# Kernel optimization log

Measured on AMD Instinct MI355X. Metric: run time of the kernel, lower is better.

Reference implementation:

```python
import jax, jax.numpy as jnp
import numpy as np

FEAT_STRIDE = 16
PRE_NMS_TOP_N = 4000   # cfg[cfg_key].RPN_PRE_NMS_TOP_N
POST_NMS_TOP_N = 300   # cfg[cfg_key].RPN_POST_NMS_TOP_N
NMS_THRESH = 0.7       # cfg[cfg_key].RPN_NMS_THRESH


def _generate_anchors(base_size=16, ratios=(0.5, 1.0, 2.0), scales=(8, 16, 32)):
    ratios = np.array(ratios, dtype=np.float64)
    scales = np.array(scales, dtype=np.float64)
    base = np.array([1, 1, base_size, base_size], dtype=np.float64) - 1

    def whctrs(a):
        w = a[2] - a[0] + 1
        h = a[3] - a[1] + 1
        return w, h, a[0] + 0.5 * (w - 1), a[1] + 0.5 * (h - 1)

    def mk(ws, hs, xc, yc):
        ws = np.atleast_1d(ws)[:, None]
        hs = np.atleast_1d(hs)[:, None]
        return np.hstack((xc - 0.5 * (ws - 1), yc - 0.5 * (hs - 1),
                          xc + 0.5 * (ws - 1), yc + 0.5 * (hs - 1)))

    w, h, xc, yc = whctrs(base)
    size = w * h
    ws = np.round(np.sqrt(size / ratios))
    hs = np.round(ws * ratios)
    ratio_anchors = mk(ws, hs, xc, yc)
    out = []
    for i in range(ratio_anchors.shape[0]):
        w, h, xc, yc = whctrs(ratio_anchors[i])
        out.append(mk(w * scales, h * scales, xc, yc))
    return np.vstack(out).astype(np.float32)  # [9,4]


def _nms_keep(boxes, thresh):
    # boxes sorted by score desc, [N,4]; torchvision-style IoU (no +1).
    x1, y1, x2, y2 = boxes[:, 0], boxes[:, 1], boxes[:, 2], boxes[:, 3]
    areas = (x2 - x1) * (y2 - y1)
    lt = jnp.maximum(boxes[:, None, :2], boxes[None, :, :2])
    rb = jnp.minimum(boxes[:, None, 2:], boxes[None, :, 2:])
    wh = jnp.clip(rb - lt, 0.0)
    inter = wh[..., 0] * wh[..., 1]
    iou = inter / (areas[:, None] + areas[None, :] - inter + 1e-9)  # [N,N]
    N = boxes.shape[0]
    idx = jnp.arange(N)
    def body(i, keep):
        sup = (iou[i] > thresh) & (idx > i) & keep[i]
        return keep & ~sup
    return jax.lax.fori_loop(0, N, body, jnp.ones((N,), jnp.bool_))


def _per_image(boxes, scores):
    # pre-NMS top-k by score (matches sort-desc + slice)
    _, order = jax.lax.top_k(scores, PRE_NMS_TOP_N)
    b = boxes[order]
    keep = _nms_keep(jax.lax.stop_gradient(b), NMS_THRESH)
    rank = jnp.cumsum(keep) - 1                       # position among kept
    tgt = jnp.where(keep, rank, POST_NMS_TOP_N)       # OOB indices are dropped
    return jnp.zeros((POST_NMS_TOP_N, 4), boxes.dtype).at[tgt].set(b, mode='drop')


def reference(scores, bbox_deltas, im_info, anchors):
    B, A, H, W = scores.shape
    # anchor shifts over the feature grid
    sx = jnp.arange(W, dtype=scores.dtype) * FEAT_STRIDE
    sy = jnp.arange(H, dtype=scores.dtype) * FEAT_STRIDE
    yy, xx = jnp.meshgrid(sy, sx, indexing='ij')
    shifts = jnp.stack([xx.ravel(), yy.ravel(), xx.ravel(), yy.ravel()], axis=1)  # [K,4]
    all_anchors = (anchors[None, :, :] + shifts[:, None, :]).reshape(-1, 4)       # [K*A,4]

    deltas = bbox_deltas.transpose(0, 2, 3, 1).reshape(B, -1, 4)  # [B,K*A,4]
    sc = scores.transpose(0, 2, 3, 1).reshape(B, -1)              # [B,K*A]

    # bbox_transform_inv
    w = all_anchors[:, 2] - all_anchors[:, 0] + 1.0
    h = all_anchors[:, 3] - all_anchors[:, 1] + 1.0
    cx = all_anchors[:, 0] + 0.5 * w
    cy = all_anchors[:, 1] + 0.5 * h
    pcx = deltas[..., 0] * w + cx
    pcy = deltas[..., 1] * h + cy
    pw = jnp.exp(deltas[..., 2]) * w
    ph = jnp.exp(deltas[..., 3]) * h
    props = jnp.stack([pcx - 0.5 * pw, pcy - 0.5 * ph,
                       pcx + 0.5 * pw, pcy + 0.5 * ph], axis=-1)  # [B,K*A,4]

    # clip_boxes: x in [0, im_w-1], y in [0, im_h-1]
    hi = jnp.stack([im_info[:, 1] - 1, im_info[:, 0] - 1,
                    im_info[:, 1] - 1, im_info[:, 0] - 1], axis=1)  # [B,4]
    props = jnp.clip(props, 0.0, hi[:, None, :])

    boxes_out = jax.vmap(_per_image)(props, sc)  # [B,POST,4]
    batch_col = jnp.broadcast_to(
        jnp.arange(B, dtype=scores.dtype)[:, None, None], (B, POST_NMS_TOP_N, 1))
    return jnp.concatenate([batch_col, boxes_out], axis=-1)  # [B,POST,5]


def setup_inputs():
    key = jax.random.key(0)
    k1, k2 = jax.random.split(key)
    B, A, H, W = 4, 9, 50, 76
    scores = jax.random.normal(k1, (B, A, H, W), jnp.float32)
    bbox_deltas = jax.random.normal(k2, (B, 4 * A, H, W), jnp.float32) * 0.2
    im_info = jnp.tile(jnp.array([[800.0, 1216.0, 1.0]], jnp.float32), (B, 1))
    anchors = jnp.asarray(_generate_anchors())
    return {"scores": scores, "bbox_deltas": bbox_deltas,
            "im_info": im_info, "anchors": anchors}
```

## Files before the change

### kernel.cpp

```cpp
#include <hip/hip_runtime.h>
#include <stdint.h>

#define A_N 9
#define H_N 50
#define W_N 76
#define HW_N (H_N * W_N)
#define N_PROP (A_N * HW_N)
#define B_N 4
#define PRE_NMS 4000
#define POST_NMS 300
#define NMS_TH 0.7f
#define SORT_N 4096
#define MASK_WORDS 64
#define CAND_MAX 5120
#define NBINS 4096
#define NPAIR 32
#define NLW 5
#define DEC_BLKS ((N_PROP + 255) / 256)

__global__ __launch_bounds__(256) void decode_kernel(
    const float* __restrict__ scores,
    const float* __restrict__ deltas,
    const float* __restrict__ im_info,
    const float* __restrict__ anchors,
    float4* __restrict__ boxes,
    unsigned long long* __restrict__ keys,
    unsigned* __restrict__ ghist) {
#pragma clang fp contract(off)
    __shared__ unsigned hist[NBINS];
    int tid = threadIdx.x;
    int b = blockIdx.y;
    int r = blockIdx.x * 256 + tid;
#pragma unroll
    for (int i = 0; i < NBINS / 256; ++i) hist[tid + i * 256] = 0u;
    __syncthreads();

    if (r < N_PROP) {
        int a = r / HW_N;
        int hw = r - a * HW_N;
        int hy = hw / W_N;
        int wx = hw - hy * W_N;

        float sx = (float)wx * 16.0f;
        float sy = (float)hy * 16.0f;
        float ax1 = anchors[a * 4 + 0] + sx;
        float ay1 = anchors[a * 4 + 1] + sy;
        float ax2 = anchors[a * 4 + 2] + sx;
        float ay2 = anchors[a * 4 + 3] + sy;
        float aw = ax2 - ax1 + 1.0f;
        float ah = ay2 - ay1 + 1.0f;
        float cx = ax1 + 0.5f * aw;
        float cy = ay1 + 0.5f * ah;

        const float* db = deltas + ((size_t)b * 36 + (size_t)a * 4) * HW_N + hw;
        float d0 = db[0];
        float d1 = db[HW_N];
        float d2 = db[2 * HW_N];
        float d3 = db[3 * HW_N];

        float pcx = d0 * aw + cx;
        float pcy = d1 * ah + cy;
        float pw  = expf(d2) * aw;
        float ph  = expf(d3) * ah;

        float x1 = pcx - 0.5f * pw;
        float y1 = pcy - 0.5f * ph;
        float x2 = pcx + 0.5f * pw;
        float y2 = pcy + 0.5f * ph;

        float xhi = im_info[b * 3 + 1] - 1.0f;
        float yhi = im_info[b * 3 + 0] - 1.0f;
        x1 = fminf(fmaxf(x1, 0.0f), xhi);
        y1 = fminf(fmaxf(y1, 0.0f), yhi);
        x2 = fminf(fmaxf(x2, 0.0f), xhi);
        y2 = fminf(fmaxf(y2, 0.0f), yhi);

        boxes[(size_t)b * N_PROP + r] = make_float4(x1, y1, x2, y2);

        float s = scores[((size_t)b * A_N + a) * HW_N + hw];
        unsigned f = __float_as_uint(s);
        unsigned sk = f ^ ((f & 0x80000000u) ? 0xFFFFFFFFu : 0x80000000u);
        unsigned n_ref = (unsigned)(hw * A_N + a);
        unsigned long long key = ((unsigned long long)sk << 32) | (unsigned)(~n_ref);
        keys[(size_t)b * N_PROP + r] = key;
        atomicAdd(&hist[(unsigned)(key >> 52)], 1u);
    }
    __syncthreads();
#pragma unroll
    for (int i = 0; i < NBINS / 256; ++i) {
        unsigned v = hist[tid + i * 256];
        if (v) atomicAdd(&ghist[b * NBINS + tid + i * 256], v);
    }
}

__global__ __launch_bounds__(64) void findT_kernel(const unsigned* __restrict__ ghist,
                                                   int* __restrict__ Tout) {
    __shared__ unsigned h[NBINS];
    int b = blockIdx.x;
    int lane = threadIdx.x;
    for (int i = lane; i < NBINS; i += 64) h[i] = ghist[b * NBINS + i];
    __syncthreads();
    unsigned gsum = 0;
    for (int j = 0; j < 64; ++j) gsum += h[lane * 64 + j];
    unsigned s = gsum;
    for (int d = 1; d < 64; d <<= 1) {
        unsigned t = (unsigned)__shfl_down((int)s, d);
        if (lane + d < 64) s += t;
    }
    unsigned long long bal = __ballot(s >= PRE_NMS);
    int gstar = 63 - __builtin_clzll(bal);
    unsigned after = (gstar < 63) ? (unsigned)__builtin_amdgcn_readlane((int)s, gstar + 1) : 0u;
    unsigned R = PRE_NMS - after;
    unsigned s2 = h[gstar * 64 + lane];
    for (int d = 1; d < 64; d <<= 1) {
        unsigned t = (unsigned)__shfl_down((int)s2, d);
        if (lane + d < 64) s2 += t;
    }
    unsigned long long bal2 = __ballot(s2 >= R);
    int j = 63 - __builtin_clzll(bal2);
    if (lane == 0) Tout[b] = gstar * 64 + j;
}

__global__ void compact_kernel(const unsigned long long* __restrict__ keys,
                               const int* __restrict__ T,
                               unsigned* __restrict__ cnt,
                               unsigned long long* __restrict__ cand) {
    int b = blockIdx.y;
    int n = blockIdx.x * 256 + threadIdx.x;
    bool pred = false;
    unsigned long long k = 0ull;
    if (n < N_PROP) {
        k = keys[(size_t)b * N_PROP + n];
        pred = ((int)(unsigned)(k >> 52) >= T[b]);
    }
    unsigned long long m = __ballot(pred);
    if (m) {
        int lane = threadIdx.x & 63;
        int lead = __ffsll((unsigned long long)m) - 1;
        unsigned base = 0;
        if (lane == lead) base = atomicAdd(&cnt[b], (unsigned)__popcll(m));
        base = __shfl((int)base, lead);
        if (pred) {
            unsigned pos = base + (unsigned)__popcll(m & ((1ull << lane) - 1ull));
            if (pos < CAND_MAX) cand[(size_t)b * CAND_MAX + pos] = k;
        }
    }
}

__global__ __launch_bounds__(256) void rank_scatter_kernel(
    const unsigned long long* __restrict__ cand,
    const unsigned* __restrict__ cnt,
    const float4* __restrict__ boxes,
    float4* __restrict__ sortedBoxes) {
    __shared__ unsigned long long sk[256];
    int b = blockIdx.y;
    int tid = threadIdx.x;
    int ci = blockIdx.x * 64 + (tid >> 2);
    int q = tid & 3;
    int mc = (int)min(cnt[b], (unsigned)CAND_MAX);
    unsigned long long my = (ci < mc) ? cand[(size_t)b * CAND_MAX + ci] : 0ull;
    int rank = 0;
    int nt = (mc + 255) >> 8;
    for (int t = 0; t < nt; ++t) {
        int j = t * 256 + tid;
        sk[tid] = (j < mc) ? cand[(size_t)b * CAND_MAX + j] : 0ull;
        __syncthreads();
#pragma unroll 16
        for (int c = 0; c < 64; ++c) {
            int cc = q * 64 + ((c + q * 17) & 63);
            rank += (sk[cc] > my) ? 1 : 0;
        }
        __syncthreads();
    }
    rank += __shfl_xor(rank, 1);
    rank += __shfl_xor(rank, 2);
    if (q == 0 && ci < mc && rank < PRE_NMS) {
        unsigned n_ref = ~(unsigned)(my & 0xFFFFFFFFull);
        unsigned a = n_ref % A_N;
        unsigned hw = n_ref / A_N;
        sortedBoxes[(size_t)b * SORT_N + rank] =
            boxes[(size_t)b * N_PROP + a * HW_N + hw];
    }
    if (q == 1) {
        int pi = blockIdx.x * 64 + (tid >> 2);
        if (pi >= PRE_NMS && pi < SORT_N)
            sortedBoxes[(size_t)b * SORT_N + pi] = make_float4(0.f, 0.f, 0.f, 0.f);
    }
}

__global__ __launch_bounds__(256) void iou_mask_kernel(
    const float4* __restrict__ sortedBoxes,
    unsigned long long* __restrict__ colmaj,
    unsigned long long* __restrict__ rowmaj) {
#pragma clang fp contract(off)
    int b = blockIdx.y;
    int wv = threadIdx.x >> 6;
    int t = threadIdx.x & 63;
    int k = blockIdx.x * 4 + wv;
    int rc = 0;
    while (k >= 64 - rc) { k -= 64 - rc; ++rc; }
    int cc = rc + k;

    __shared__ float4 colb[4][64];
    colb[wv][t] = sortedBoxes[(size_t)b * SORT_N + cc * 64 + t];
    __syncthreads();

    int r = rc * 64 + t;
    float4 rb = sortedBoxes[(size_t)b * SORT_N + r];
    float rarea = (rb.z - rb.x) * (rb.w - rb.y);
    unsigned long long word = 0ull;
    for (int c = 0; c < 64; ++c) {
        int j = cc * 64 + c;
        float4 cb = colb[wv][c];
        float carea = (cb.z - cb.x) * (cb.w - cb.y);
        float ltx = fmaxf(rb.x, cb.x);
        float lty = fmaxf(rb.y, cb.y);
        float rbx = fminf(rb.z, cb.z);
        float rby = fminf(rb.w, cb.w);
        float iw = fmaxf(rbx - ltx, 0.0f);
        float ih = fmaxf(rby - lty, 0.0f);
        float inter = iw * ih;
        float iou = inter / (rarea + carea - inter + 1e-9f);
        if (iou > NMS_TH && j > r) word |= (1ull << c);
    }
    colmaj[((size_t)b * MASK_WORDS + cc) * SORT_N + r] = word;
    rowmaj[((size_t)b * SORT_N + r) * MASK_WORDS + cc] = word;
}

__device__ __forceinline__ unsigned long long rl64(unsigned long long v, int src) {
    unsigned lo = (unsigned)__builtin_amdgcn_readlane((int)(unsigned)(v & 0xFFFFFFFFull), src);
    unsigned hi = (unsigned)__builtin_amdgcn_readlane((int)(unsigned)(v >> 32), src);
    return ((unsigned long long)hi << 32) | lo;
}

__device__ __forceinline__ unsigned long long redor64(unsigned long long alive,
                                                      unsigned long long v, int lane) {
    unsigned long long x = ((alive >> lane) & 1ull) ? v : 0ull;
    x |= __shfl_xor(x, 1);
    x |= __shfl_xor(x, 2);
    x |= __shfl_xor(x, 4);
    x |= __shfl_xor(x, 8);
    x |= __shfl_xor(x, 16);
    x |= __shfl_xor(x, 32);
    return x;
}

__device__ __forceinline__ void block_sync() {
    asm volatile("s_waitcnt lgkmcnt(0)" ::: "memory");
    __builtin_amdgcn_s_barrier();
    asm volatile("" ::: "memory");
}

#define GLOAD(dst, addr) \
    asm volatile("global_load_dwordx2 %0, %1, off" : "=v"(dst) : "v"(addr))
#define WAITV0 asm volatile("s_waitcnt vmcnt(0)" ::: "memory")
#define SCHED0 __builtin_amdgcn_sched_barrier(0)

#define TILE_COL(P, t) ((t) < 6 ? 2 * (P) + (t) : 2 * (P) + 1 + ((t) - 6))
#define TILE_RB(P, t)  ((size_t)((t) < 6 ? 2 * (P) : 2 * (P) + 1) << 6)
#define TILE_ADDR(P, t) \
    (C + (size_t)(TILE_COL(P, t) < 64 ? TILE_COL(P, t) : 63) * SORT_N + TILE_RB(P, t) + lane)

#define ISSUE_PAIR(P)                                                          \
    do {                                                                       \
        pf_vmask = 0u;                                                         \
        GLOAD(pf0,  TILE_ADDR(P, 0));  if (TILE_COL(P, 0)  < 64) pf_vmask |= 1u << 0;  \
        GLOAD(pf1,  TILE_ADDR(P, 1));  if (TILE_COL(P, 1)  < 64) pf_vmask |= 1u << 1;  \
        GLOAD(pf2,  TILE_ADDR(P, 2));  if (TILE_COL(P, 2)  < 64) pf_vmask |= 1u << 2;  \
        GLOAD(pf3,  TILE_ADDR(P, 3));  if (TILE_COL(P, 3)  < 64) pf_vmask |= 1u << 3;  \
        GLOAD(pf4,  TILE_ADDR(P, 4));  if (TILE_COL(P, 4)  < 64) pf_vmask |= 1u << 4;  \
        GLOAD(pf5,  TILE_ADDR(P, 5));  if (TILE_COL(P, 5)  < 64) pf_vmask |= 1u << 5;  \
        GLOAD(pf6,  TILE_ADDR(P, 6));  if (TILE_COL(P, 6)  < 64) pf_vmask |= 1u << 6;  \
        GLOAD(pf7,  TILE_ADDR(P, 7));  if (TILE_COL(P, 7)  < 64) pf_vmask |= 1u << 7;  \
        GLOAD(pf8,  TILE_ADDR(P, 8));  if (TILE_COL(P, 8)  < 64) pf_vmask |= 1u << 8;  \
        GLOAD(pf9,  TILE_ADDR(P, 9));  if (TILE_COL(P, 9)  < 64) pf_vmask |= 1u << 9;  \
        GLOAD(pf10, TILE_ADDR(P, 10)); if (TILE_COL(P, 10) < 64) pf_vmask |= 1u << 10; \
    } while (0)

#define NEXTROW2(rk)                                                           \
    int rk;                                                                    \
    {                                                                          \
        if (xA) { int bb_ = __builtin_ctzll(xA); xA &= xA - 1; rk = baseA + bb_; } \
        else if (xB) { int bb_ = __builtin_ctzll(xB); xB &= xB - 1; rk = baseB + bb_; } \
        else rk = rpad;                                                        \
    }

__global__ __launch_bounds__(512, 1) void nms_scan_kernel(
    const unsigned long long* __restrict__ colmaj,
    const unsigned long long* __restrict__ rowmaj,
    const float4* __restrict__ sortedBoxes,
    float* __restrict__ out) {
    int b = blockIdx.x;
    int tid = threadIdx.x;
    int lane = tid & 63;
    int wv = tid >> 6;
    const unsigned long long* C = colmaj + (size_t)b * MASK_WORDS * SORT_N;
    const unsigned long long* R = rowmaj + (size_t)b * SORT_N * MASK_WORDS;

    __shared__ int kept[POST_NMS];
    __shared__ unsigned remW[MASK_WORDS][2];
    __shared__ unsigned long long aliveLds[MASK_WORDS];
    __shared__ unsigned long long ring[4][11][64];
    __shared__ unsigned long long car2[2][2];
    __shared__ int doneLds;
    __shared__ int kcntLds;

    if (tid < MASK_WORDS) { remW[tid][0] = 0u; remW[tid][1] = 0u; aliveLds[tid] = 0ull; }
    if (tid < 4) car2[tid >> 1][tid & 1] = 0ull;
    if (tid == 0) { doneLds = 0; kcntLds = 0; }

    unsigned long long pf0=0,pf1=0,pf2=0,pf3=0,pf4=0,pf5=0,pf6=0,pf7=0,pf8=0,pf9=0,pf10=0;
    unsigned pf_vmask = 0u;
    bool pf_have = false;
    unsigned long long gp0=0,gp1=0,gp2=0,gp3=0,gp4=0,gp5=0,gp6=0,gp7=0;
    bool ld_valid = false;

    if (wv == 1) {
        for (int t = 0; t < 11; ++t) {
            int col = TILE_COL(0, t);
            unsigned long long v =
                (col < 64) ? C[(size_t)col * SORT_N + TILE_RB(0, t) + lane] : 0ull;
            ring[0][t][lane] = v;
        }
        ISSUE_PAIR(1);
        pf_have = true;
    }
    block_sync();

    unsigned long long carA = 0ull, carB = 0ull;
    int kcnt = 0;

    for (int q = 0; q < NPAIR; ++q) {
        if (wv == 0) {
            int A = 2 * q, Bg = A + 1, slot = q & 3;
            unsigned long long dA  = ring[slot][0][lane];
            unsigned long long tA1 = ring[slot][1][lane];
            unsigned long long tA2 = ring[slot][2][lane];
            unsigned long long tA3 = ring[slot][3][lane];
            unsigned long long dB  = ring[slot][6][lane];
            unsigned long long tB1 = ring[slot][7][lane];
            unsigned long long tB2 = ring[slot][8][lane];
            unsigned long long remA =
                ((unsigned long long)remW[A][1] << 32) | (unsigned long long)remW[A][0];
            unsigned long long remB =
                ((unsigned long long)remW[Bg][1] << 32) | (unsigned long long)remW[Bg][0];
            unsigned long long h2A = car2[q & 1][0];
            unsigned long long h2B = car2[q & 1][1];
            bool hit = false;
            unsigned long long aliveA = 0ull, aliveB = 0ull;
            unsigned long long pend = ~(remA | carA | h2A);
            while (pend) {
                int bit = __builtin_ctzll(pend);
                if (lane == 0) kept[kcnt] = (A << 6) + bit;
                ++kcnt;
                aliveA |= 1ull << bit;
                if (kcnt == POST_NMS) { hit = true; break; }
                pend &= ~(rl64(dA, bit) | (1ull << bit));
            }
            if (!hit) {
                unsigned long long nA1 = redor64(aliveA, tA1, lane);
                pend = ~(remB | carB | h2B | nA1);
                while (pend) {
                    int bit = __builtin_ctzll(pend);
                    if (lane == 0) kept[kcnt] = (Bg << 6) + bit;
                    ++kcnt;
                    aliveB |= 1ull << bit;
                    if (kcnt == POST_NMS) { hit = true; break; }
                    pend &= ~(rl64(dB, bit) | (1ull << bit));
                }
            }
            carA = redor64(aliveA, tA2, lane) | redor64(aliveB, tB1, lane);
            carB = redor64(aliveA, tA3, lane) | redor64(aliveB, tB2, lane);
            if (lane == 0) {
                aliveLds[A]  = aliveA;
                aliveLds[Bg] = aliveB;
                kcntLds = kcnt;
                if (hit) doneLds = 1;
            }
        } else if (wv == 1) {
            if (pf_have) {
                WAITV0;
                SCHED0;
                int wp = q + 1;
                if (wp < NPAIR) {
                    int ws = wp & 3;
                    ring[ws][0][lane]  = (pf_vmask & (1u << 0))  ? pf0  : 0ull;
                    ring[ws][1][lane]  = (pf_vmask & (1u << 1))  ? pf1  : 0ull;
                    ring[ws][2][lane]  = (pf_vmask & (1u << 2))  ? pf2  : 0ull;
                    ring[ws][3][lane]  = (pf_vmask & (1u << 3))  ? pf3  : 0ull;
                    ring[ws][4][lane]  = (pf_vmask & (1u << 4))  ? pf4  : 0ull;
                    ring[ws][5][lane]  = (pf_vmask & (1u << 5))  ? pf5  : 0ull;
                    ring[ws][6][lane]  = (pf_vmask & (1u << 6))  ? pf6  : 0ull;
                    ring[ws][7][lane]  = (pf_vmask & (1u << 7))  ? pf7  : 0ull;
                    ring[ws][8][lane]  = (pf_vmask & (1u << 8))  ? pf8  : 0ull;
                    ring[ws][9][lane]  = (pf_vmask & (1u << 9))  ? pf9  : 0ull;
                    ring[ws][10][lane] = (pf_vmask & (1u << 10)) ? pf10 : 0ull;
                }
                pf_have = false;
            }
            int ip = q + 2;
            if (ip < NPAIR) {
                ISSUE_PAIR(ip);
                pf_have = true;
            }
        } else if (wv == 2) {
            if (q >= 1) {
                int p = q - 1, sp = p & 3;
                unsigned long long aA = aliveLds[2 * p];
                unsigned long long aB = aliveLds[2 * p + 1];
                unsigned long long tA4 = ring[sp][4][lane];
                unsigned long long tA5 = ring[sp][5][lane];
                unsigned long long tB3 = ring[sp][9][lane];
                unsigned long long tB4 = ring[sp][10][lane];
                unsigned long long c0 = redor64(aA, tA4, lane) | redor64(aB, tB3, lane);
                unsigned long long c1 = redor64(aA, tA5, lane) | redor64(aB, tB4, lane);
                if (lane == 0) {
                    car2[(q + 1) & 1][0] = c0;
                    car2[(q + 1) & 1][1] = c1;
                }
            }
        } else {
            if (ld_valid) {
                WAITV0;
                SCHED0;
                unsigned long long acc =
                    ((gp0 | gp1) | (gp2 | gp3)) | ((gp4 | gp5) | (gp6 | gp7));
                unsigned lo = (unsigned)acc, hi = (unsigned)(acc >> 32);
                if (lo) atomicOr(&remW[lane][0], lo);
                if (hi) atomicOr(&remW[lane][1], hi);
                ld_valid = false;
            }
            if (q >= 1) {
                int p = q - 1, gA = 2 * p, gB = 2 * p + 1;
                unsigned long long aA = aliveLds[gA];
                unsigned long long aB = aliveLds[gB];
                int k = wv - 3;
                unsigned long long below = (1ull << lane) - 1ull;
                bool inA = (aA >> lane) & 1ull;
                bool inB = (aB >> lane) & 1ull;
                int posA = (int)__popcll(aA & below);
                int posB = (int)__popcll(aA) + (int)__popcll(aB & below);
                unsigned long long mA = __ballot(inA && (posA % NLW) == k);
                unsigned long long mB = __ballot(inB && (posB % NLW) == k);
                if (mA | mB) {
                    int baseA = gA << 6, baseB = gB << 6;
                    unsigned long long xA = mA, xB = mB;
                    int rpad = mA ? (baseA + __builtin_ctzll(mA))
                                  : (baseB + __builtin_ctzll(mB));
                    NEXTROW2(r0) NEXTROW2(r1) NEXTROW2(r2) NEXTROW2(r3)
                    NEXTROW2(r4) NEXTROW2(r5) NEXTROW2(r6) NEXTROW2(r7)
                    const unsigned long long* Rb = R + lane;
                    GLOAD(gp0, Rb + (size_t)r0 * MASK_WORDS);
                    GLOAD(gp1, Rb + (size_t)r1 * MASK_WORDS);
                    GLOAD(gp2, Rb + (size_t)r2 * MASK_WORDS);
                    GLOAD(gp3, Rb + (size_t)r3 * MASK_WORDS);
                    GLOAD(gp4, Rb + (size_t)r4 * MASK_WORDS);
                    GLOAD(gp5, Rb + (size_t)r5 * MASK_WORDS);
                    GLOAD(gp6, Rb + (size_t)r6 * MASK_WORDS);
                    GLOAD(gp7, Rb + (size_t)r7 * MASK_WORDS);
                    ld_valid = true;
                    unsigned long long ovf = 0ull;
                    while (xA) {
                        int bb = __builtin_ctzll(xA); xA &= xA - 1;
                        ovf |= Rb[(size_t)(baseA + bb) * MASK_WORDS];
                    }
                    while (xB) {
                        int bb = __builtin_ctzll(xB); xB &= xB - 1;
                        ovf |= Rb[(size_t)(baseB + bb) * MASK_WORDS];
                    }
                    if (ovf) {
                        unsigned lo = (unsigned)ovf, hi = (unsigned)(ovf >> 32);
                        if (lo) atomicOr(&remW[lane][0], lo);
                        if (hi) atomicOr(&remW[lane][1], hi);
                    }
                }
            }
        }
        block_sync();
        if (doneLds) break;
    }

    WAITV0;
    __syncthreads();

    int kc = kcntLds;
    for (int r = tid; r < POST_NMS; r += 512) {
        float* o = out + ((size_t)b * POST_NMS + r) * 5;
        float4 bx = make_float4(0.f, 0.f, 0.f, 0.f);
        if (r < kc) bx = sortedBoxes[(size_t)b * SORT_N + kept[r]];
        o[0] = (float)b;
        o[1] = bx.x;
        o[2] = bx.y;
        o[3] = bx.z;
        o[4] = bx.w;
    }
}

extern "C" void kernel_launch(void* const* d_in, const int* in_sizes, int n_in,
                              void* d_out, int out_size, void* d_ws, size_t ws_size,
                              hipStream_t stream) {
    const float* scores  = (const float*)d_in[0];
    const float* deltas  = (const float*)d_in[1];
    const float* im_info = (const float*)d_in[2];
    const float* anchors = (const float*)d_in[3];
    float* out = (float*)d_out;

    char* ws = (char*)d_ws;
    size_t off = 0;
    float4* boxes = (float4*)(ws + off);
    off += (size_t)B_N * N_PROP * sizeof(float4);
    off = (off + 255) & ~(size_t)255;
    unsigned long long* keys = (unsigned long long*)(ws + off);
    off += (size_t)B_N * N_PROP * sizeof(unsigned long long);
    off = (off + 255) & ~(size_t)255;
    float4* sortedBoxes = (float4*)(ws + off);
    off += (size_t)B_N * SORT_N * sizeof(float4);
    off = (off + 255) & ~(size_t)255;
    unsigned long long* colmaj = (unsigned long long*)(ws + off);
    off += (size_t)B_N * MASK_WORDS * SORT_N * sizeof(unsigned long long);
    off = (off + 255) & ~(size_t)255;
    unsigned long long* rowmaj = (unsigned long long*)(ws + off);
    off += (size_t)B_N * SORT_N * MASK_WORDS * sizeof(unsigned long long);
    off = (off + 255) & ~(size_t)255;
    unsigned long long* cand = (unsigned long long*)(ws + off);
    off += (size_t)B_N * CAND_MAX * sizeof(unsigned long long);
    off = (off + 255) & ~(size_t)255;
    unsigned* ghist = (unsigned*)(ws + off);
    size_t zero_off = off;
    off += (size_t)B_N * NBINS * sizeof(unsigned);
    unsigned* cnt = (unsigned*)(ws + off);
    off += (size_t)B_N * sizeof(unsigned);
    size_t zero_bytes = off - zero_off;
    off = (off + 255) & ~(size_t)255;
    int* Tbuf = (int*)(ws + off);
    off += (size_t)B_N * sizeof(int);

    hipMemsetAsync((void*)ghist, 0, zero_bytes, stream);

    decode_kernel<<<dim3(DEC_BLKS, B_N), 256, 0, stream>>>(
        scores, deltas, im_info, anchors, boxes, keys, ghist);
    findT_kernel<<<B_N, 64, 0, stream>>>(ghist, Tbuf);
    compact_kernel<<<dim3((N_PROP + 255) / 256, B_N), 256, 0, stream>>>(
        keys, Tbuf, cnt, cand);
    rank_scatter_kernel<<<dim3(CAND_MAX / 64, B_N), 256, 0, stream>>>(
        cand, cnt, boxes, sortedBoxes);
    iou_mask_kernel<<<dim3(520, B_N), 256, 0, stream>>>(sortedBoxes, colmaj, rowmaj);
    nms_scan_kernel<<<B_N, 512, 0, stream>>>(colmaj, rowmaj, sortedBoxes, out);
}
```

Before: 214.5 us.

## Fuse all pipeline stages into one cooperative persistent kernel with grid syncs

```diff
diff --git a/kernel.cpp b/kernel.cpp
--- a/kernel.cpp
+++ b/kernel.cpp
@@ -1,5 +1,8 @@
 #include <hip/hip_runtime.h>
+#include <hip/hip_cooperative_groups.h>
 #include <stdint.h>
+
+namespace cg = cooperative_groups;
 
 #define A_N 9
 #define H_N 50
@@ -15,217 +18,9 @@
 #define CAND_MAX 5120
 #define NBINS 4096
 #define NPAIR 32
-#define NLW 5
 #define DEC_BLKS ((N_PROP + 255) / 256)
-
-__global__ __launch_bounds__(256) void decode_kernel(
-    const float* __restrict__ scores,
-    const float* __restrict__ deltas,
-    const float* __restrict__ im_info,
-    const float* __restrict__ anchors,
-    float4* __restrict__ boxes,
-    unsigned long long* __restrict__ keys,
-    unsigned* __restrict__ ghist) {
-#pragma clang fp contract(off)
-    __shared__ unsigned hist[NBINS];
-    int tid = threadIdx.x;
-    int b = blockIdx.y;
-    int r = blockIdx.x * 256 + tid;
-#pragma unroll
-    for (int i = 0; i < NBINS / 256; ++i) hist[tid + i * 256] = 0u;
-    __syncthreads();
-
-    if (r < N_PROP) {
-        int a = r / HW_N;
-        int hw = r - a * HW_N;
-        int hy = hw / W_N;
-        int wx = hw - hy * W_N;
-
-        float sx = (float)wx * 16.0f;
-        float sy = (float)hy * 16.0f;
-        float ax1 = anchors[a * 4 + 0] + sx;
-        float ay1 = anchors[a * 4 + 1] + sy;
-        float ax2 = anchors[a * 4 + 2] + sx;
-        float ay2 = anchors[a * 4 + 3] + sy;
-        float aw = ax2 - ax1 + 1.0f;
-        float ah = ay2 - ay1 + 1.0f;
-        float cx = ax1 + 0.5f * aw;
-        float cy = ay1 + 0.5f * ah;
-
-        const float* db = deltas + ((size_t)b * 36 + (size_t)a * 4) * HW_N + hw;
-        float d0 = db[0];
-        float d1 = db[HW_N];
-        float d2 = db[2 * HW_N];
-        float d3 = db[3 * HW_N];
-
-        float pcx = d0 * aw + cx;
-        float pcy = d1 * ah + cy;
-        float pw  = expf(d2) * aw;
-        float ph  = expf(d3) * ah;
-
-        float x1 = pcx - 0.5f * pw;
-        float y1 = pcy - 0.5f * ph;
-        float x2 = pcx + 0.5f * pw;
-        float y2 = pcy + 0.5f * ph;
-
-        float xhi = im_info[b * 3 + 1] - 1.0f;
-        float yhi = im_info[b * 3 + 0] - 1.0f;
-        x1 = fminf(fmaxf(x1, 0.0f), xhi);
-        y1 = fminf(fmaxf(y1, 0.0f), yhi);
-        x2 = fminf(fmaxf(x2, 0.0f), xhi);
-        y2 = fminf(fmaxf(y2, 0.0f), yhi);
-
-        boxes[(size_t)b * N_PROP + r] = make_float4(x1, y1, x2, y2);
-
-        float s = scores[((size_t)b * A_N + a) * HW_N + hw];
-        unsigned f = __float_as_uint(s);
-        unsigned sk = f ^ ((f & 0x80000000u) ? 0xFFFFFFFFu : 0x80000000u);
-        unsigned n_ref = (unsigned)(hw * A_N + a);
-        unsigned long long key = ((unsigned long long)sk << 32) | (unsigned)(~n_ref);
-        keys[(size_t)b * N_PROP + r] = key;
-        atomicAdd(&hist[(unsigned)(key >> 52)], 1u);
-    }
-    __syncthreads();
-#pragma unroll
-    for (int i = 0; i < NBINS / 256; ++i) {
-        unsigned v = hist[tid + i * 256];
-        if (v) atomicAdd(&ghist[b * NBINS + tid + i * 256], v);
-    }
-}
-
-__global__ __launch_bounds__(64) void findT_kernel(const unsigned* __restrict__ ghist,
-                                                   int* __restrict__ Tout) {
-    __shared__ unsigned h[NBINS];
-    int b = blockIdx.x;
-    int lane = threadIdx.x;
-    for (int i = lane; i < NBINS; i += 64) h[i] = ghist[b * NBINS + i];
-    __syncthreads();
-    unsigned gsum = 0;
-    for (int j = 0; j < 64; ++j) gsum += h[lane * 64 + j];
-    unsigned s = gsum;
-    for (int d = 1; d < 64; d <<= 1) {
-        unsigned t = (unsigned)__shfl_down((int)s, d);
-        if (lane + d < 64) s += t;
-    }
-    unsigned long long bal = __ballot(s >= PRE_NMS);
-    int gstar = 63 - __builtin_clzll(bal);
-    unsigned after = (gstar < 63) ? (unsigned)__builtin_amdgcn_readlane((int)s, gstar + 1) : 0u;
-    unsigned R = PRE_NMS - after;
-    unsigned s2 = h[gstar * 64 + lane];
-    for (int d = 1; d < 64; d <<= 1) {
-        unsigned t = (unsigned)__shfl_down((int)s2, d);
-        if (lane + d < 64) s2 += t;
-    }
-    unsigned long long bal2 = __ballot(s2 >= R);
-    int j = 63 - __builtin_clzll(bal2);
-    if (lane == 0) Tout[b] = gstar * 64 + j;
-}
-
-__global__ void compact_kernel(const unsigned long long* __restrict__ keys,
-                               const int* __restrict__ T,
-                               unsigned* __restrict__ cnt,
-                               unsigned long long* __restrict__ cand) {
-    int b = blockIdx.y;
-    int n = blockIdx.x * 256 + threadIdx.x;
-    bool pred = false;
-    unsigned long long k = 0ull;
-    if (n < N_PROP) {
-        k = keys[(size_t)b * N_PROP + n];
-        pred = ((int)(unsigned)(k >> 52) >= T[b]);
-    }
-    unsigned long long m = __ballot(pred);
-    if (m) {
-        int lane = threadIdx.x & 63;
-        int lead = __ffsll((unsigned long long)m) - 1;
-        unsigned base = 0;
-        if (lane == lead) base = atomicAdd(&cnt[b], (unsigned)__popcll(m));
-        base = __shfl((int)base, lead);
-        if (pred) {
-            unsigned pos = base + (unsigned)__popcll(m & ((1ull << lane) - 1ull));
-            if (pos < CAND_MAX) cand[(size_t)b * CAND_MAX + pos] = k;
-        }
-    }
-}
-
-__global__ __launch_bounds__(256) void rank_scatter_kernel(
-    const unsigned long long* __restrict__ cand,
-    const unsigned* __restrict__ cnt,
-    const float4* __restrict__ boxes,
-    float4* __restrict__ sortedBoxes) {
-    __shared__ unsigned long long sk[256];
-    int b = blockIdx.y;
-    int tid = threadIdx.x;
-    int ci = blockIdx.x * 64 + (tid >> 2);
-    int q = tid & 3;
-    int mc = (int)min(cnt[b], (unsigned)CAND_MAX);
-    unsigned long long my = (ci < mc) ? cand[(size_t)b * CAND_MAX + ci] : 0ull;
-    int rank = 0;
-    int nt = (mc + 255) >> 8;
-    for (int t = 0; t < nt; ++t) {
-        int j = t * 256 + tid;
-        sk[tid] = (j < mc) ? cand[(size_t)b * CAND_MAX + j] : 0ull;
-        __syncthreads();
-#pragma unroll 16
-        for (int c = 0; c < 64; ++c) {
-            int cc = q * 64 + ((c + q * 17) & 63);
-            rank += (sk[cc] > my) ? 1 : 0;
-        }
-        __syncthreads();
-    }
-    rank += __shfl_xor(rank, 1);
-    rank += __shfl_xor(rank, 2);
-    if (q == 0 && ci < mc && rank < PRE_NMS) {
-        unsigned n_ref = ~(unsigned)(my & 0xFFFFFFFFull);
-        unsigned a = n_ref % A_N;
-        unsigned hw = n_ref / A_N;
-        sortedBoxes[(size_t)b * SORT_N + rank] =
-            boxes[(size_t)b * N_PROP + a * HW_N + hw];
-    }
-    if (q == 1) {
-        int pi = blockIdx.x * 64 + (tid >> 2);
-        if (pi >= PRE_NMS && pi < SORT_N)
-            sortedBoxes[(size_t)b * SORT_N + pi] = make_float4(0.f, 0.f, 0.f, 0.f);
-    }
-}
-
-__global__ __launch_bounds__(256) void iou_mask_kernel(
-    const float4* __restrict__ sortedBoxes,
-    unsigned long long* __restrict__ colmaj,
-    unsigned long long* __restrict__ rowmaj) {
-#pragma clang fp contract(off)
-    int b = blockIdx.y;
-    int wv = threadIdx.x >> 6;
-    int t = threadIdx.x & 63;
-    int k = blockIdx.x * 4 + wv;
-    int rc = 0;
-    while (k >= 64 - rc) { k -= 64 - rc; ++rc; }
-    int cc = rc + k;
-
-    __shared__ float4 colb[4][64];
-    colb[wv][t] = sortedBoxes[(size_t)b * SORT_N + cc * 64 + t];
-    __syncthreads();
-
-    int r = rc * 64 + t;
-    float4 rb = sortedBoxes[(size_t)b * SORT_N + r];
-    float rarea = (rb.z - rb.x) * (rb.w - rb.y);
-    unsigned long long word = 0ull;
-    for (int c = 0; c < 64; ++c) {
-        int j = cc * 64 + c;
-        float4 cb = colb[wv][c];
-        float carea = (cb.z - cb.x) * (cb.w - cb.y);
-        float ltx = fmaxf(rb.x, cb.x);
-        float lty = fmaxf(rb.y, cb.y);
-        float rbx = fminf(rb.z, cb.z);
-        float rby = fminf(rb.w, cb.w);
-        float iw = fmaxf(rbx - ltx, 0.0f);
-        float ih = fmaxf(rby - lty, 0.0f);
-        float inter = iw * ih;
-        float iou = inter / (rarea + carea - inter + 1e-9f);
-        if (iou > NMS_TH && j > r) word |= (1ull << c);
-    }
-    colmaj[((size_t)b * MASK_WORDS + cc) * SORT_N + r] = word;
-    rowmaj[((size_t)b * SORT_N + r) * MASK_WORDS + cc] = word;
-}
+#define GRID_BLKS 512
+#define TILES_PB 2080
 
 __device__ __forceinline__ unsigned long long rl64(unsigned long long v, int src) {
     unsigned lo = (unsigned)__builtin_amdgcn_readlane((int)(unsigned)(v & 0xFFFFFFFFull), src);
@@ -285,214 +80,441 @@
         else rk = rpad;                                                        \
     }
 
-__global__ __launch_bounds__(512, 1) void nms_scan_kernel(
-    const unsigned long long* __restrict__ colmaj,
-    const unsigned long long* __restrict__ rowmaj,
-    const float4* __restrict__ sortedBoxes,
+#define FOLD_GP()                                                              \
+    do {                                                                       \
+        unsigned long long acc =                                               \
+            ((gp0 | gp1) | (gp2 | gp3)) | ((gp4 | gp5) | (gp6 | gp7));         \
+        unsigned lo = (unsigned)acc, hi = (unsigned)(acc >> 32);               \
+        if (lo) atomicOr(&remW[lane * 2 + 0], lo);                             \
+        if (hi) atomicOr(&remW[lane * 2 + 1], hi);                             \
+    } while (0)
+
+#define LOADER_ISSUE(KK)                                                       \
+    if (q >= 1) {                                                              \
+        int p_ = q - 1, gA = 2 * p_, gB = 2 * p_ + 1;                          \
+        unsigned long long aA = aliveLds[gA];                                  \
+        unsigned long long aB = aliveLds[gB];                                  \
+        unsigned long long below = (1ull << lane) - 1ull;                      \
+        bool inA = (aA >> lane) & 1ull;                                        \
+        bool inB = (aB >> lane) & 1ull;                                        \
+        int posA = (int)__popcll(aA & below);                                  \
+        int posB = (int)__popcll(aA) + (int)__popcll(aB & below);              \
+        unsigned long long mA = __ballot(inA && (posA % 3) == (KK));           \
+        unsigned long long mB = __ballot(inB && (posB % 3) == (KK));           \
+        if (mA | mB) {                                                         \
+            int baseA = gA << 6, baseB = gB << 6;                              \
+            unsigned long long xA = mA, xB = mB;                               \
+            int rpad = mA ? (baseA + __builtin_ctzll(mA))                      \
+                          : (baseB + __builtin_ctzll(mB));                     \
+            NEXTROW2(r0) NEXTROW2(r1) NEXTROW2(r2) NEXTROW2(r3)                \
+            NEXTROW2(r4) NEXTROW2(r5) NEXTROW2(r6) NEXTROW2(r7)                \
+            const unsigned long long* Rb = R + lane;                           \
+            GLOAD(gp0, Rb + (size_t)r0 * MASK_WORDS);                          \
+            GLOAD(gp1, Rb + (size_t)r1 * MASK_WORDS);                          \
+            GLOAD(gp2, Rb + (size_t)r2 * MASK_WORDS);                          \
+            GLOAD(gp3, Rb + (size_t)r3 * MASK_WORDS);                          \
+            GLOAD(gp4, Rb + (size_t)r4 * MASK_WORDS);                          \
+            GLOAD(gp5, Rb + (size_t)r5 * MASK_WORDS);                          \
+            GLOAD(gp6, Rb + (size_t)r6 * MASK_WORDS);                          \
+            GLOAD(gp7, Rb + (size_t)r7 * MASK_WORDS);                          \
+            ld_valid = true;                                                   \
+            unsigned long long ovf = 0ull;                                     \
+            while (xA) {                                                       \
+                int bb = __builtin_ctzll(xA); xA &= xA - 1;                    \
+                ovf |= Rb[(size_t)(baseA + bb) * MASK_WORDS];                  \
+            }                                                                  \
+            while (xB) {                                                       \
+                int bb = __builtin_ctzll(xB); xB &= xB - 1;                    \
+                ovf |= Rb[(size_t)(baseB + bb) * MASK_WORDS];                  \
+            }                                                                  \
+            if (ovf) {                                                         \
+                unsigned lo = (unsigned)ovf, hi = (unsigned)(ovf >> 32);       \
+                if (lo) atomicOr(&remW[lane * 2 + 0], lo);                     \
+                if (hi) atomicOr(&remW[lane * 2 + 1], hi);                     \
+            }                                                                  \
+        }                                                                      \
+    }
+
+__global__ __launch_bounds__(256) void fused_kernel(
+    const float* __restrict__ scores,
+    const float* __restrict__ deltas,
+    const float* __restrict__ im_info,
+    const float* __restrict__ anchors,
+    float4* __restrict__ boxes,
+    unsigned long long* __restrict__ keys,
+    unsigned* __restrict__ ghist,
+    unsigned* __restrict__ cnt,
+    unsigned long long* __restrict__ cand,
+    float4* __restrict__ sortedBoxes,
+    unsigned long long* __restrict__ colmaj,
+    unsigned long long* __restrict__ rowmaj,
     float* __restrict__ out) {
-    int b = blockIdx.x;
-    int tid = threadIdx.x;
-    int lane = tid & 63;
-    int wv = tid >> 6;
-    const unsigned long long* C = colmaj + (size_t)b * MASK_WORDS * SORT_N;
-    const unsigned long long* R = rowmaj + (size_t)b * SORT_N * MASK_WORDS;
-
-    __shared__ int kept[POST_NMS];
-    __shared__ unsigned remW[MASK_WORDS][2];
-    __shared__ unsigned long long aliveLds[MASK_WORDS];
-    __shared__ unsigned long long ring[4][11][64];
-    __shared__ unsigned long long car2[2][2];
-    __shared__ int doneLds;
-    __shared__ int kcntLds;
-
-    if (tid < MASK_WORDS) { remW[tid][0] = 0u; remW[tid][1] = 0u; aliveLds[tid] = 0ull; }
-    if (tid < 4) car2[tid >> 1][tid & 1] = 0ull;
-    if (tid == 0) { doneLds = 0; kcntLds = 0; }
-
-    unsigned long long pf0=0,pf1=0,pf2=0,pf3=0,pf4=0,pf5=0,pf6=0,pf7=0,pf8=0,pf9=0,pf10=0;
-    unsigned pf_vmask = 0u;
-    bool pf_have = false;
-    unsigned long long gp0=0,gp1=0,gp2=0,gp3=0,gp4=0,gp5=0,gp6=0,gp7=0;
-    bool ld_valid = false;
-
-    if (wv == 1) {
-        for (int t = 0; t < 11; ++t) {
-            int col = TILE_COL(0, t);
-            unsigned long long v =
-                (col < 64) ? C[(size_t)col * SORT_N + TILE_RB(0, t) + lane] : 0ull;
-            ring[0][t][lane] = v;
-        }
-        ISSUE_PAIR(1);
-        pf_have = true;
-    }
-    block_sync();
-
-    unsigned long long carA = 0ull, carB = 0ull;
-    int kcnt = 0;
-
-    for (int q = 0; q < NPAIR; ++q) {
-        if (wv == 0) {
-            int A = 2 * q, Bg = A + 1, slot = q & 3;
-            unsigned long long dA  = ring[slot][0][lane];
-            unsigned long long tA1 = ring[slot][1][lane];
-            unsigned long long tA2 = ring[slot][2][lane];
-            unsigned long long tA3 = ring[slot][3][lane];
-            unsigned long long dB  = ring[slot][6][lane];
-            unsigned long long tB1 = ring[slot][7][lane];
-            unsigned long long tB2 = ring[slot][8][lane];
-            unsigned long long remA =
-                ((unsigned long long)remW[A][1] << 32) | (unsigned long long)remW[A][0];
-            unsigned long long remB =
-                ((unsigned long long)remW[Bg][1] << 32) | (unsigned long long)remW[Bg][0];
-            unsigned long long h2A = car2[q & 1][0];
-            unsigned long long h2B = car2[q & 1][1];
-            bool hit = false;
-            unsigned long long aliveA = 0ull, aliveB = 0ull;
-            unsigned long long pend = ~(remA | carA | h2A);
-            while (pend) {
-                int bit = __builtin_ctzll(pend);
-                if (lane == 0) kept[kcnt] = (A << 6) + bit;
-                ++kcnt;
-                aliveA |= 1ull << bit;
-                if (kcnt == POST_NMS) { hit = true; break; }
-                pend &= ~(rl64(dA, bit) | (1ull << bit));
-            }
-            if (!hit) {
-                unsigned long long nA1 = redor64(aliveA, tA1, lane);
-                pend = ~(remB | carB | h2B | nA1);
+#pragma clang fp contract(off)
+    cg::grid_group grid = cg::this_grid();
+    __shared__ __align__(16) unsigned long long SMEM[3104];
+    const int tid = threadIdx.x;
+    const int bid = blockIdx.x;
+
+    {
+        int i = bid * 256 + tid;
+        if (i < B_N * NBINS) ghist[i] = 0u;
+        if (bid == 0 && tid < B_N) cnt[tid] = 0u;
+    }
+    grid.sync();
+
+    {
+        unsigned* hist = (unsigned*)SMEM;
+        for (int vt = bid; vt < B_N * DEC_BLKS; vt += GRID_BLKS) {
+            __syncthreads();
+#pragma unroll
+            for (int i2 = 0; i2 < NBINS / 256; ++i2) hist[tid + i2 * 256] = 0u;
+            __syncthreads();
+            int b = vt / DEC_BLKS;
+            int r = (vt - b * DEC_BLKS) * 256 + tid;
+            if (r < N_PROP) {
+                int a = r / HW_N;
+                int hw = r - a * HW_N;
+                int hy = hw / W_N;
+                int wx = hw - hy * W_N;
+
+                float sx = (float)wx * 16.0f;
+                float sy = (float)hy * 16.0f;
+                float ax1 = anchors[a * 4 + 0] + sx;
+                float ay1 = anchors[a * 4 + 1] + sy;
+                float ax2 = anchors[a * 4 + 2] + sx;
+                float ay2 = anchors[a * 4 + 3] + sy;
+                float aw = ax2 - ax1 + 1.0f;
+                float ah = ay2 - ay1 + 1.0f;
+                float cx = ax1 + 0.5f * aw;
+                float cy = ay1 + 0.5f * ah;
+
+                const float* db = deltas + ((size_t)b * 36 + (size_t)a * 4) * HW_N + hw;
+                float d0 = db[0];
+                float d1 = db[HW_N];
+                float d2 = db[2 * HW_N];
+                float d3 = db[3 * HW_N];
+
+                float pcx = d0 * aw + cx;
+                float pcy = d1 * ah + cy;
+                float pw  = expf(d2) * aw;
+                float ph  = expf(d3) * ah;
+
+                float x1 = pcx - 0.5f * pw;
+                float y1 = pcy - 0.5f * ph;
+                float x2 = pcx + 0.5f * pw;
+                float y2 = pcy + 0.5f * ph;
+
+                float xhi = im_info[b * 3 + 1] - 1.0f;
+                float yhi = im_info[b * 3 + 0] - 1.0f;
+                x1 = fminf(fmaxf(x1, 0.0f), xhi);
+                y1 = fminf(fmaxf(y1, 0.0f), yhi);
+                x2 = fminf(fmaxf(x2, 0.0f), xhi);
+                y2 = fminf(fmaxf(y2, 0.0f), yhi);
+
+                boxes[(size_t)b * N_PROP + r] = make_float4(x1, y1, x2, y2);
+
+                float s = scores[((size_t)b * A_N + a) * HW_N + hw];
+                unsigned f = __float_as_uint(s);
+                unsigned sk2 = f ^ ((f & 0x80000000u) ? 0xFFFFFFFFu : 0x80000000u);
+                unsigned n_ref = (unsigned)(hw * A_N + a);
+                unsigned long long key =
+                    ((unsigned long long)sk2 << 32) | (unsigned)(~n_ref);
+                keys[(size_t)b * N_PROP + r] = key;
+                atomicAdd(&hist[(unsigned)(key >> 52)], 1u);
+            }
+            __syncthreads();
+#pragma unroll
+            for (int i2 = 0; i2 < NBINS / 256; ++i2) {
+                unsigned v = hist[tid + i2 * 256];
+                if (v) atomicAdd(&ghist[b * NBINS + tid + i2 * 256], v);
+            }
+        }
+    }
+    grid.sync();
+
+    {
+        int* Ts = (int*)SMEM;
+        if (tid < 64) {
+            for (int b = 0; b < B_N; ++b) {
+                unsigned gsum = 0;
+                for (int j = 0; j < 64; ++j) gsum += ghist[b * NBINS + tid * 64 + j];
+                unsigned s = gsum;
+                for (int d = 1; d < 64; d <<= 1) {
+                    unsigned t = (unsigned)__shfl_down((int)s, d);
+                    if (tid + d < 64) s += t;
+                }
+                unsigned long long bal = __ballot(s >= PRE_NMS);
+                int gstar = 63 - __builtin_clzll(bal);
+                unsigned after = (gstar < 63)
+                    ? (unsigned)__builtin_amdgcn_readlane((int)s, gstar + 1) : 0u;
+                unsigned Rr = PRE_NMS - after;
+                unsigned s2 = ghist[b * NBINS + gstar * 64 + tid];
+                for (int d = 1; d < 64; d <<= 1) {
+                    unsigned t = (unsigned)__shfl_down((int)s2, d);
+                    if (tid + d < 64) s2 += t;
+                }
+                unsigned long long bal2 = __ballot(s2 >= Rr);
+                int j = 63 - __builtin_clzll(bal2);
+                if (tid == 0) Ts[b] = gstar * 64 + j;
+            }
+        }
+        __syncthreads();
+        int T0 = Ts[0], T1 = Ts[1], T2 = Ts[2], T3 = Ts[3];
+        for (int vt = bid; vt < B_N * DEC_BLKS; vt += GRID_BLKS) {
+            int b = vt / DEC_BLKS;
+            int Tb = (b == 0) ? T0 : (b == 1) ? T1 : (b == 2) ? T2 : T3;
+            int n = (vt - b * DEC_BLKS) * 256 + tid;
+            bool pred = false;
+            unsigned long long k = 0ull;
+            if (n < N_PROP) {
+                k = keys[(size_t)b * N_PROP + n];
+                pred = ((int)(unsigned)(k >> 52) >= Tb);
+            }
+            unsigned long long m = __ballot(pred);
+            if (m) {
+                int lane = tid & 63;
+                int lead = __ffsll((unsigned long long)m) - 1;
+                unsigned base = 0;
+                if (lane == lead) base = atomicAdd(&cnt[b], (unsigned)__popcll(m));
+                base = __shfl((int)base, lead);
+                if (pred) {
+                    unsigned pos = base + (unsigned)__popcll(m & ((1ull << lane) - 1ull));
+                    if (pos < CAND_MAX) cand[(size_t)b * CAND_MAX + pos] = k;
+                }
+            }
+        }
+    }
+    grid.sync();
+
+    if (bid < 80 * B_N) {
+        unsigned long long* sk = SMEM;
+        int b = bid / 80;
+        int cblk = bid - b * 80;
+        int ci = cblk * 64 + (tid >> 2);
+        int qq = tid & 3;
+        int mc = (int)min(cnt[b], (unsigned)CAND_MAX);
+        unsigned long long my = (ci < mc) ? cand[(size_t)b * CAND_MAX + ci] : 0ull;
+        int rank = 0;
+        int nt = (mc + 255) >> 8;
+        for (int t = 0; t < nt; ++t) {
+            int j = t * 256 + tid;
+            sk[tid] = (j < mc) ? cand[(size_t)b * CAND_MAX + j] : 0ull;
+            __syncthreads();
+#pragma unroll 16
+            for (int c = 0; c < 64; ++c) {
+                int cc = qq * 64 + ((c + qq * 17) & 63);
+                rank += (sk[cc] > my) ? 1 : 0;
+            }
+            __syncthreads();
+        }
+        rank += __shfl_xor(rank, 1);
+        rank += __shfl_xor(rank, 2);
+        if (qq == 0 && ci < mc && rank < PRE_NMS) {
+            unsigned n_ref = ~(unsigned)(my & 0xFFFFFFFFull);
+            unsigned a = n_ref % A_N;
+            unsigned hw = n_ref / A_N;
+            sortedBoxes[(size_t)b * SORT_N + rank] =
+                boxes[(size_t)b * N_PROP + a * HW_N + hw];
+        }
+        if (qq == 1) {
+            int pi = cblk * 64 + (tid >> 2);
+            if (pi >= PRE_NMS && pi < SORT_N)
+                sortedBoxes[(size_t)b * SORT_N + pi] = make_float4(0.f, 0.f, 0.f, 0.f);
+        }
+    }
+    grid.sync();
+
+    {
+        int wvv = tid >> 6, t64 = tid & 63;
+        float4* colb = (float4*)SMEM + wvv * 64;
+        for (int t = 0; t < 5; ++t) {
+            int lin = bid * 4 + wvv + t * (GRID_BLKS * 4);
+            if (lin >= B_N * TILES_PB) break;
+            int b = lin / TILES_PB;
+            int k = lin - b * TILES_PB;
+            int rc = 0;
+            while (k >= 64 - rc) { k -= 64 - rc; ++rc; }
+            int cc = rc + k;
+            colb[t64] = sortedBoxes[(size_t)b * SORT_N + cc * 64 + t64];
+            int r = rc * 64 + t64;
+            float4 rb = sortedBoxes[(size_t)b * SORT_N + r];
+            float rarea = (rb.z - rb.x) * (rb.w - rb.y);
+            unsigned long long word = 0ull;
+            for (int c = 0; c < 64; ++c) {
+                int j = cc * 64 + c;
+                float4 cb = colb[c];
+                float carea = (cb.z - cb.x) * (cb.w - cb.y);
+                float ltx = fmaxf(rb.x, cb.x);
+                float lty = fmaxf(rb.y, cb.y);
+                float rbx = fminf(rb.z, cb.z);
+                float rby = fminf(rb.w, cb.w);
+                float iw = fmaxf(rbx - ltx, 0.0f);
+                float ih = fmaxf(rby - lty, 0.0f);
+                float inter = iw * ih;
+                float iou = inter / (rarea + carea - inter + 1e-9f);
+                if (iou > NMS_TH && j > r) word |= (1ull << c);
+            }
+            colmaj[((size_t)b * MASK_WORDS + cc) * SORT_N + r] = word;
+            rowmaj[((size_t)b * SORT_N + r) * MASK_WORDS + cc] = word;
+        }
+    }
+    grid.sync();
+
+    if (bid < B_N) {
+        const int b = bid;
+        const int lane = tid & 63;
+        const int wv = tid >> 6;
+        const unsigned long long* C = colmaj + (size_t)b * MASK_WORDS * SORT_N;
+        const unsigned long long* R = rowmaj + (size_t)b * SORT_N * MASK_WORDS;
+
+        unsigned long long (*ring)[64] =
+            reinterpret_cast<unsigned long long (*)[64]>(SMEM);
+        unsigned long long* aliveLds = SMEM + 2816;
+        unsigned long long* car2v = SMEM + 2880;
+        unsigned* remW = (unsigned*)(SMEM + 2884);
+        int* kept = (int*)(SMEM + 2948);
+        int* flagsI = (int*)(SMEM + 3098);
+
+        if (tid < MASK_WORDS) {
+            remW[tid * 2] = 0u; remW[tid * 2 + 1] = 0u; aliveLds[tid] = 0ull;
+        }
+        if (tid < 4) car2v[tid] = 0ull;
+        if (tid == 0) { flagsI[0] = 0; flagsI[1] = 0; }
+
+        unsigned long long pf0=0,pf1=0,pf2=0,pf3=0,pf4=0,pf5=0,pf6=0,pf7=0,pf8=0,pf9=0,pf10=0;
+        unsigned pf_vmask = 0u;
+        bool pf_have = false;
+        unsigned long long gp0=0,gp1=0,gp2=0,gp3=0,gp4=0,gp5=0,gp6=0,gp7=0;
+        bool ld_valid = false;
+
+        if (wv == 1) {
+            for (int t = 0; t < 11; ++t) {
+                int col = TILE_COL(0, t);
+                unsigned long long v =
+                    (col < 64) ? C[(size_t)col * SORT_N + TILE_RB(0, t) + lane] : 0ull;
+                ring[t][lane] = v;
+            }
+            ISSUE_PAIR(1);
+            pf_have = true;
+        }
+        block_sync();
+
+        unsigned long long carA = 0ull, carB = 0ull;
+        int kcnt = 0;
+
+        for (int q = 0; q < NPAIR; ++q) {
+            if (wv == 0) {
+                int A = 2 * q, Bg = A + 1, slot = q & 3;
+                unsigned long long dA  = ring[slot * 11 + 0][lane];
+                unsigned long long tA1 = ring[slot * 11 + 1][lane];
+                unsigned long long tA2 = ring[slot * 11 + 2][lane];
+                unsigned long long tA3 = ring[slot * 11 + 3][lane];
+                unsigned long long dB  = ring[slot * 11 + 6][lane];
+                unsigned long long tB1 = ring[slot * 11 + 7][lane];
+                unsigned long long tB2 = ring[slot * 11 + 8][lane];
+                unsigned long long remA =
+                    ((unsigned long long)remW[A * 2 + 1] << 32) |
+                    (unsigned long long)remW[A * 2 + 0];
+                unsigned long long remB =
+                    ((unsigned long long)remW[Bg * 2 + 1] << 32) |
+                    (unsigned long long)remW[Bg * 2 + 0];
+                unsigned long long h2A = car2v[(q & 1) * 2 + 0];
+                unsigned long long h2B = car2v[(q & 1) * 2 + 1];
+                bool hit = false;
+                unsigned long long aliveA = 0ull, aliveB = 0ull;
+                unsigned long long pend = ~(remA | carA | h2A);
                 while (pend) {
                     int bit = __builtin_ctzll(pend);
-                    if (lane == 0) kept[kcnt] = (Bg << 6) + bit;
+                    if (lane == 0) kept[kcnt] = (A << 6) + bit;
                     ++kcnt;
-                    aliveB |= 1ull << bit;
+                    aliveA |= 1ull << bit;
                     if (kcnt == POST_NMS) { hit = true; break; }
-                    pend &= ~(rl64(dB, bit) | (1ull << bit));
-                }
-            }
-            carA = redor64(aliveA, tA2, lane) | redor64(aliveB, tB1, lane);
-            carB = redor64(aliveA, tA3, lane) | redor64(aliveB, tB2, lane);
-            if (lane == 0) {
-                aliveLds[A]  = aliveA;
-                aliveLds[Bg] = aliveB;
-                kcntLds = kcnt;
-                if (hit) doneLds = 1;
-            }
-        } else if (wv == 1) {
-            if (pf_have) {
-                WAITV0;
-                SCHED0;
-                int wp = q + 1;
-                if (wp < NPAIR) {
-                    int ws = wp & 3;
-                    ring[ws][0][lane]  = (pf_vmask & (1u << 0))  ? pf0  : 0ull;
-                    ring[ws][1][lane]  = (pf_vmask & (1u << 1))  ? pf1  : 0ull;
-                    ring[ws][2][lane]  = (pf_vmask & (1u << 2))  ? pf2  : 0ull;
-                    ring[ws][3][lane]  = (pf_vmask & (1u << 3))  ? pf3  : 0ull;
-                    ring[ws][4][lane]  = (pf_vmask & (1u << 4))  ? pf4  : 0ull;
-                    ring[ws][5][lane]  = (pf_vmask & (1u << 5))  ? pf5  : 0ull;
-                    ring[ws][6][lane]  = (pf_vmask & (1u << 6))  ? pf6  : 0ull;
-                    ring[ws][7][lane]  = (pf_vmask & (1u << 7))  ? pf7  : 0ull;
-                    ring[ws][8][lane]  = (pf_vmask & (1u << 8))  ? pf8  : 0ull;
-                    ring[ws][9][lane]  = (pf_vmask & (1u << 9))  ? pf9  : 0ull;
-                    ring[ws][10][lane] = (pf_vmask & (1u << 10)) ? pf10 : 0ull;
-                }
-                pf_have = false;
-            }
-            int ip = q + 2;
-            if (ip < NPAIR) {
-                ISSUE_PAIR(ip);
-                pf_have = true;
-            }
-        } else if (wv == 2) {
-            if (q >= 1) {
-                int p = q - 1, sp = p & 3;
-                unsigned long long aA = aliveLds[2 * p];
-                unsigned long long aB = aliveLds[2 * p + 1];
-                unsigned long long tA4 = ring[sp][4][lane];
-                unsigned long long tA5 = ring[sp][5][lane];
-                unsigned long long tB3 = ring[sp][9][lane];
-                unsigned long long tB4 = ring[sp][10][lane];
-                unsigned long long c0 = redor64(aA, tA4, lane) | redor64(aB, tB3, lane);
-                unsigned long long c1 = redor64(aA, tA5, lane) | redor64(aB, tB4, lane);
+                    pend &= ~(rl64(dA, bit) | (1ull << bit));
+                }
+                if (!hit) {
+                    unsigned long long nA1 = redor64(aliveA, tA1, lane);
+                    pend = ~(remB | carB | h2B | nA1);
+                    while (pend) {
+                        int bit = __builtin_ctzll(pend);
+                        if (lane == 0) kept[kcnt] = (Bg << 6) + bit;
+                        ++kcnt;
+                        aliveB |= 1ull << bit;
+                        if (kcnt == POST_NMS) { hit = true; break; }
+                        pend &= ~(rl64(dB, bit) | (1ull << bit));
+                    }
+                }
+                carA = redor64(aliveA, tA2, lane) | redor64(aliveB, tB1, lane);
+                carB = redor64(aliveA, tA3, lane) | redor64(aliveB, tB2, lane);
                 if (lane == 0) {
-                    car2[(q + 1) & 1][0] = c0;
-                    car2[(q + 1) & 1][1] = c1;
-                }
-            }
-        } else {
-            if (ld_valid) {
-                WAITV0;
-                SCHED0;
-                unsigned long long acc =
-                    ((gp0 | gp1) | (gp2 | gp3)) | ((gp4 | gp5) | (gp6 | gp7));
-                unsigned lo = (unsigned)acc, hi = (unsigned)(acc >> 32);
-                if (lo) atomicOr(&remW[lane][0], lo);
-                if (hi) atomicOr(&remW[lane][1], hi);
-                ld_valid = false;
-            }
-            if (q >= 1) {
-                int p = q - 1, gA = 2 * p, gB = 2 * p + 1;
-                unsigned long long aA = aliveLds[gA];
-                unsigned long long aB = aliveLds[gB];
-                int k = wv - 3;
-                unsigned long long below = (1ull << lane) - 1ull;
-                bool inA = (aA >> lane) & 1ull;
-                bool inB = (aB >> lane) & 1ull;
-                int posA = (int)__popcll(aA & below);
-                int posB = (int)__popcll(aA) + (int)__popcll(aB & below);
-                unsigned long long mA = __ballot(inA && (posA % NLW) == k);
-                unsigned long long mB = __ballot(inB && (posB % NLW) == k);
-                if (mA | mB) {
-                    int baseA = gA << 6, baseB = gB << 6;
-                    unsigned long long xA = mA, xB = mB;
-                    int rpad = mA ? (baseA + __builtin_ctzll(mA))
-                                  : (baseB + __builtin_ctzll(mB));
-                    NEXTROW2(r0) NEXTROW2(r1) NEXTROW2(r2) NEXTROW2(r3)
-                    NEXTROW2(r4) NEXTROW2(r5) NEXTROW2(r6) NEXTROW2(r7)
-                    const unsigned long long* Rb = R + lane;
-                    GLOAD(gp0, Rb + (size_t)r0 * MASK_WORDS);
-                    GLOAD(gp1, Rb + (size_t)r1 * MASK_WORDS);
-                    GLOAD(gp2, Rb + (size_t)r2 * MASK_WORDS);
-                    GLOAD(gp3, Rb + (size_t)r3 * MASK_WORDS);
-                    GLOAD(gp4, Rb + (size_t)r4 * MASK_WORDS);
-                    GLOAD(gp5, Rb + (size_t)r5 * MASK_WORDS);
-                    GLOAD(gp6, Rb + (size_t)r6 * MASK_WORDS);
-                    GLOAD(gp7, Rb + (size_t)r7 * MASK_WORDS);
-                    ld_valid = true;
-                    unsigned long long ovf = 0ull;
-                    while (xA) {
-                        int bb = __builtin_ctzll(xA); xA &= xA - 1;
-                        ovf |= Rb[(size_t)(baseA + bb) * MASK_WORDS];
+                    aliveLds[A]  = aliveA;
+                    aliveLds[Bg] = aliveB;
+                    flagsI[1] = kcnt;
+                    if (hit) flagsI[0] = 1;
+                }
+            } else if (wv == 1) {
+                if (pf_have || ld_valid) { WAITV0; SCHED0; }
+                if (pf_have) {
+                    int wp = q + 1;
+                    if (wp < NPAIR) {
+                        int ws = wp & 3;
+                        ring[ws * 11 + 0][lane]  = (pf_vmask & (1u << 0))  ? pf0  : 0ull;
+                        ring[ws * 11 + 1][lane]  = (pf_vmask & (1u << 1))  ? pf1  : 0ull;
+                        ring[ws * 11 + 2][lane]  = (pf_vmask & (1u << 2))  ? pf2  : 0ull;
+                        ring[ws * 11 + 3][lane]  = (pf_vmask & (1u << 3))  ? pf3  : 0ull;
+                        ring[ws * 11 + 4][lane]  = (pf_vmask & (1u << 4))  ? pf4  : 0ull;
+                        ring[ws * 11 + 5][lane]  = (pf_vmask & (1u << 5))  ? pf5  : 0ull;
+                        ring[ws * 11 + 6][lane]  = (pf_vmask & (1u << 6))  ? pf6  : 0ull;
+                        ring[ws * 11 + 7][lane]  = (pf_vmask & (1u << 7))  ? pf7  : 0ull;
+                        ring[ws * 11 + 8][lane]  = (pf_vmask & (1u << 8))  ? pf8  : 0ull;
+                        ring[ws * 11 + 9][lane]  = (pf_vmask & (1u << 9))  ? pf9  : 0ull;
+                        ring[ws * 11 + 10][lane] = (pf_vmask & (1u << 10)) ? pf10 : 0ull;
                     }
-                    while (xB) {
-                        int bb = __builtin_ctzll(xB); xB &= xB - 1;
-                        ovf |= Rb[(size_t)(baseB + bb) * MASK_WORDS];
+                    pf_have = false;
+                }
+                if (ld_valid) { FOLD_GP(); ld_valid = false; }
+                int ip = q + 2;
+                if (ip < NPAIR) { ISSUE_PAIR(ip); pf_have = true; }
+                LOADER_ISSUE(2)
+            } else if (wv == 2) {
+                if (ld_valid) { WAITV0; SCHED0; FOLD_GP(); ld_valid = false; }
+                if (q >= 1) {
+                    int p = q - 1, sp = p & 3;
+                    unsigned long long aA = aliveLds[2 * p];
+                    unsigned long long aB = aliveLds[2 * p + 1];
+                    unsigned long long tA4 = ring[sp * 11 + 4][lane];
+                    unsigned long long tA5 = ring[sp * 11 + 5][lane];
+                    unsigned long long tB3 = ring[sp * 11 + 9][lane];
+                    unsigned long long tB4 = ring[sp * 11 + 10][lane];
+                    unsigned long long c0 = redor64(aA, tA4, lane) | redor64(aB, tB3, lane);
+                    unsigned long long c1 = redor64(aA, tA5, lane) | redor64(aB, tB4, lane);
+                    if (lane == 0) {
+                        car2v[((q + 1) & 1) * 2 + 0] = c0;
+                        car2v[((q + 1) & 1) * 2 + 1] = c1;
                     }
-                    if (ovf) {
-                        unsigned lo = (unsigned)ovf, hi = (unsigned)(ovf >> 32);
-                        if (lo) atomicOr(&remW[lane][0], lo);
-                        if (hi) atomicOr(&remW[lane][1], hi);
-                    }
-                }
-            }
-        }
-        block_sync();
-        if (doneLds) break;
-    }
-
-    WAITV0;
-    __syncthreads();
-
-    int kc = kcntLds;
-    for (int r = tid; r < POST_NMS; r += 512) {
-        float* o = out + ((size_t)b * POST_NMS + r) * 5;
-        float4 bx = make_float4(0.f, 0.f, 0.f, 0.f);
-        if (r < kc) bx = sortedBoxes[(size_t)b * SORT_N + kept[r]];
-        o[0] = (float)b;
-        o[1] = bx.x;
-        o[2] = bx.y;
-        o[3] = bx.z;
-        o[4] = bx.w;
+                }
+                LOADER_ISSUE(1)
+            } else {
+                if (ld_valid) { WAITV0; SCHED0; FOLD_GP(); ld_valid = false; }
+                LOADER_ISSUE(0)
+            }
+            block_sync();
+            if (flagsI[0]) break;
+        }
+
+        WAITV0;
+        __syncthreads();
+
+        int kc = flagsI[1];
+        for (int r = tid; r < POST_NMS; r += 256) {
+            float* o = out + ((size_t)b * POST_NMS + r) * 5;
+            float4 bx = make_float4(0.f, 0.f, 0.f, 0.f);
+            if (r < kc) bx = sortedBoxes[(size_t)b * SORT_N + kept[r]];
+            o[0] = (float)b;
+            o[1] = bx.x;
+            o[2] = bx.y;
+            o[3] = bx.z;
+            o[4] = bx.w;
+        }
     }
 }
 
@@ -526,24 +548,15 @@
     off += (size_t)B_N * CAND_MAX * sizeof(unsigned long long);
     off = (off + 255) & ~(size_t)255;
     unsigned* ghist = (unsigned*)(ws + off);
-    size_t zero_off = off;
     off += (size_t)B_N * NBINS * sizeof(unsigned);
     unsigned* cnt = (unsigned*)(ws + off);
     off += (size_t)B_N * sizeof(unsigned);
-    size_t zero_bytes = off - zero_off;
-    off = (off + 255) & ~(size_t)255;
-    int* Tbuf = (int*)(ws + off);
-    off += (size_t)B_N * sizeof(int);
-
-    hipMemsetAsync((void*)ghist, 0, zero_bytes, stream);
-
-    decode_kernel<<<dim3(DEC_BLKS, B_N), 256, 0, stream>>>(
-        scores, deltas, im_info, anchors, boxes, keys, ghist);
-    findT_kernel<<<B_N, 64, 0, stream>>>(ghist, Tbuf);
-    compact_kernel<<<dim3((N_PROP + 255) / 256, B_N), 256, 0, stream>>>(
-        keys, Tbuf, cnt, cand);
-    rank_scatter_kernel<<<dim3(CAND_MAX / 64, B_N), 256, 0, stream>>>(
-        cand, cnt, boxes, sortedBoxes);
-    iou_mask_kernel<<<dim3(520, B_N), 256, 0, stream>>>(sortedBoxes, colmaj, rowmaj);
-    nms_scan_kernel<<<B_N, 512, 0, stream>>>(colmaj, rowmaj, sortedBoxes, out);
+
+    void* args[] = {
+        (void*)&scores, (void*)&deltas, (void*)&im_info, (void*)&anchors,
+        (void*)&boxes, (void*)&keys, (void*)&ghist, (void*)&cnt,
+        (void*)&cand, (void*)&sortedBoxes, (void*)&colmaj, (void*)&rowmaj,
+        (void*)&out};
+    hipLaunchCooperativeKernel((const void*)fused_kernel, dim3(GRID_BLKS),
+                               dim3(256), args, 0, stream);
 }
```

After: 466.4 us. +117.5%, slower.
